# Performance work log

Measured on AMD Instinct MI355X. Metric: run time of the kernel, lower is better.

Reference implementation:

```python
import jax, jax.numpy as jnp
import numpy as np

N_NODES = 50000
N_EDGES = 800000
D_IN = 256
HID = 128
OUT = 64
NEG_SLOPE = 0.2  # PyG GATConv default leaky_relu slope
EPS = 1e-16      # PyG softmax denominator epsilon


def _gat_conv(x, src, dst, W_src, W_dst, att_src, att_dst, bias, n_nodes):
    """Single-head PyG GATConv with add_self_loops=False.
    Returns (out [N, C_out], alpha [E])."""
    h_src = x @ W_src                     # [N, C]
    h_dst = x @ W_dst                     # [N, C]
    a_src = h_src @ att_src               # [N]
    a_dst = h_dst @ att_dst               # [N]
    logits = jax.nn.leaky_relu(a_src[src] + a_dst[dst], NEG_SLOPE)  # [E]
    # segment softmax over incoming edges of each dst node
    m = jax.ops.segment_max(logits, dst, num_segments=n_nodes)      # [N]
    e = jnp.exp(logits - m[dst])                                    # [E]
    denom = jax.ops.segment_sum(e, dst, num_segments=n_nodes)       # [N]
    alpha = e / (denom[dst] + EPS)                                  # [E]
    msg = h_src[src] * alpha[:, None]                               # [E, C]
    out = jax.ops.segment_sum(msg, dst, num_segments=n_nodes) + bias
    return out, alpha


def setup_inputs() -> dict:
    key = jax.random.key(0)
    ks = jax.random.split(key, 16)
    s = 0.05
    x = jax.random.normal(ks[0], (N_NODES, D_IN), dtype=jnp.float32)
    edge_index = jax.random.randint(ks[1], (2, N_EDGES), 0, N_NODES, dtype=jnp.int64)
    return {
        "x": x,
        "edge_index": edge_index,
        "W_src1": jax.random.normal(ks[2], (D_IN, HID), jnp.float32) * s,
        "W_dst1": jax.random.normal(ks[3], (D_IN, HID), jnp.float32) * s,
        "att_src1": jax.random.normal(ks[4], (HID,), jnp.float32) * s,
        "att_dst1": jax.random.normal(ks[5], (HID,), jnp.float32) * s,
        "b1": jnp.zeros((HID,), jnp.float32),
        "W_lin1": jax.random.normal(ks[6], (D_IN, HID), jnp.float32) * s,
        "b_lin1": jnp.zeros((HID,), jnp.float32),
        "W_src2": jax.random.normal(ks[7], (HID, OUT), jnp.float32) * s,
        "W_dst2": jax.random.normal(ks[8], (HID, OUT), jnp.float32) * s,
        "att_src2": jax.random.normal(ks[9], (OUT,), jnp.float32) * s,
        "att_dst2": jax.random.normal(ks[10], (OUT,), jnp.float32) * s,
        "b2": jnp.zeros((OUT,), jnp.float32),
        "W_lin2": jax.random.normal(ks[11], (HID, OUT), jnp.float32) * s,
        "b_lin2": jnp.zeros((OUT,), jnp.float32),
    }


def reference(x, edge_index, W_src1, W_dst1, att_src1, att_dst1, b1, W_lin1, b_lin1,
              W_src2, W_dst2, att_src2, att_dst2, b2, W_lin2, b_lin2):
    src, dst = edge_index[0], edge_index[1]
    n = x.shape[0]
    h, _ = _gat_conv(x, src, dst, W_src1, W_dst1, att_src1, att_dst1, b1, n)
    h = h + x @ W_lin1 + b_lin1
    h = jax.nn.relu(h)
    out, alpha = _gat_conv(h, src, dst, W_src2, W_dst2, att_src2, att_dst2, b2, n)
    out = out + h @ W_lin2 + b_lin2
    return out, alpha
```

## Files before the change

### kernel.cpp

```cpp
#include <hip/hip_runtime.h>
#include <math.h>

#define D_IN 256
#define HID 128
#define D_OUT 64
#define NEG_SLOPE 0.2f

#define NBUCK 196
#define BCAP  5120
#define P1_EPB 8192

typedef short short8 __attribute__((ext_vector_type(8)));
typedef float floatx4 __attribute__((ext_vector_type(4)));

__device__ __forceinline__ float wave_reduce_sum(float v) {
    #pragma unroll
    for (int off = 32; off > 0; off >>= 1) v += __shfl_xor(v, off, 64);
    return v;
}
__device__ __forceinline__ int wave_scan_incl_i(int v) {
    int lane = threadIdx.x & 63;
    #pragma unroll
    for (int off = 1; off < 64; off <<= 1) {
        int t = __shfl_up(v, off, 64);
        if (lane >= off) v += t;
    }
    return v;
}

__device__ __forceinline__ short f2bf(float f) {
    unsigned u = __float_as_uint(f);
    u += 0x7fffu + ((u >> 16) & 1u);
    return (short)(u >> 16);
}
__device__ __forceinline__ unsigned pk2(float a, float b) {
    return (unsigned)(unsigned short)f2bf(a) | ((unsigned)(unsigned short)f2bf(b) << 16);
}
__device__ __forceinline__ float bflo(unsigned p) { return __uint_as_float(p << 16); }
__device__ __forceinline__ float bfhi(unsigned p) { return __uint_as_float(p & 0xffff0000u); }

__device__ void prep_body(const float* Wsrc1, const float* att_src1,
                          const float* Wdst1, const float* att_dst1,
                          const float* Wsrc2, const float* att_src2,
                          const float* Wdst2, const float* att_dst2,
                          const float* b1, const float* b_lin1,
                          const float* b2, const float* b_lin2,
                          float* v_src1, float* v_dst1, float* v_src2, float* v_dst2,
                          float* bsum1, float* bsum2) {
    int t = threadIdx.x;
    if (t < D_IN) {
        float s1 = 0.f, s2 = 0.f;
        for (int c = 0; c < HID; c++) {
            s1 += Wsrc1[t * HID + c] * att_src1[c];
            s2 += Wdst1[t * HID + c] * att_dst1[c];
        }
        v_src1[t] = s1; v_dst1[t] = s2;
    }
    if (t < HID) {
        float s1 = 0.f, s2 = 0.f;
        for (int c = 0; c < D_OUT; c++) {
            s1 += Wsrc2[t * D_OUT + c] * att_src2[c];
            s2 += Wdst2[t * D_OUT + c] * att_dst2[c];
        }
        v_src2[t] = s1; v_dst2[t] = s2;
        bsum1[t] = b1[t] + b_lin1[t];
    }
    if (t < D_OUT) bsum2[t] = b2[t] + b_lin2[t];
}

__device__ void pack_body(const float* Wa, const float* Wb, short* Wp,
                          int NTG, int NH, int total, int idx) {
    if (idx >= total) return;
    int j = idx & 7;
    int lane = (idx >> 3) & 63;
    int r = idx >> 9;
    int nt = r % NTG;
    int s = r / NTG;
    int k = s * 32 + ((lane >> 4) * 8) + j;
    int cg = nt * 16 + (lane & 15);
    const float* W = (cg < NH) ? Wa : Wb;
    int col = (cg < NH) ? cg : cg - NH;
    Wp[idx] = f2bf(W[(size_t)k * NH + col]);
}

__device__ void bucket_scatter_body(const int* __restrict__ src, const int* __restrict__ dst,
                                    int E, int* bcur, unsigned* ebuf, int blk) {
    __shared__ int hist[NBUCK];
    __shared__ int gbase[NBUCK];
    int t = threadIdx.x;
    for (int i = t; i < NBUCK; i += 256) hist[i] = 0;
    __syncthreads();
    int e0 = blk * P1_EPB;
    int e1 = e0 + P1_EPB; if (e1 > E) e1 = E;
    for (int e = e0 + t; e < e1; e += 256)
        atomicAdd(&hist[dst[e] >> 8], 1);
    __syncthreads();
    for (int i = t; i < NBUCK; i += 256) {
        gbase[i] = atomicAdd(&bcur[i], hist[i]);
        hist[i] = 0;
    }
    __syncthreads();
    for (int e = e0 + t; e < e1; e += 256) {
        int d = dst[e];
        int b = d >> 8;
        int slot = atomicAdd(&hist[b], 1);
        int pos = gbase[b] + slot;
        if (pos < BCAP)
            ebuf[(size_t)b * BCAP + pos] = (unsigned)src[e] | ((unsigned)(d & 255) << 16);
    }
}

__global__ void fused_pre(const int* __restrict__ src, const int* __restrict__ dst, int E,
                          int* bcur, unsigned* ebuf, int P1B,
                          const float* W_src1, const float* W_lin1, short* Wp1,
                          const float* W_src2, const float* W_lin2, short* Wp2,
                          const float* att_src1, const float* W_dst1, const float* att_dst1,
                          const float* att_src2, const float* W_dst2, const float* att_dst2,
                          const float* b1, const float* b_lin1,
                          const float* b2, const float* b_lin2,
                          float* v_src1, float* v_dst1, float* v_src2, float* v_dst2,
                          float* bsum1, float* bsum2) {
    int bid = blockIdx.x;
    if (bid < P1B) {
        bucket_scatter_body(src, dst, E, bcur, ebuf, bid);
    } else if (bid < P1B + 256) {
        pack_body(W_src1, W_lin1, Wp1, 16, HID, 8 * 16 * 512, (bid - P1B) * 256 + threadIdx.x);
    } else if (bid < P1B + 320) {
        pack_body(W_src2, W_lin2, Wp2, 8, D_OUT, 4 * 8 * 512, (bid - P1B - 256) * 256 + threadIdx.x);
    } else {
        prep_body(W_src1, att_src1, W_dst1, att_dst1, W_src2, att_src2, W_dst2, att_dst2,
                  b1, b_lin1, b2, b_lin2, v_src1, v_dst1, v_src2, v_dst2, bsum1, bsum2);
    }
}

__device__ void build_csr_body(const int* __restrict__ bcur, const unsigned* __restrict__ ebuf,
                               int* __restrict__ ssrc, int* __restrict__ row_beg,
                               int* __restrict__ row_end, int Nn, int b) {
    __shared__ int cnt[256];
    __shared__ int ofs[256];
    __shared__ int wsum[4];
    int t = threadIdx.x;
    cnt[t] = 0;
    __syncthreads();
    int n = bcur[b]; if (n > BCAP) n = BCAP;
    const unsigned* eb = ebuf + (size_t)b * BCAP;
    for (int i = t; i < n; i += 256)
        atomicAdd(&cnt[eb[i] >> 16], 1);
    __syncthreads();
    int v = cnt[t];
    int incl = wave_scan_incl_i(v);
    if ((t & 63) == 63) wsum[t >> 6] = incl;
    __syncthreads();
    int add = 0;
    #pragma unroll
    for (int w = 0; w < 4; w++) if (w < (t >> 6)) add += wsum[w];
    int excl = add + incl - v;
    int base = b * BCAP;
    int node = b * 256 + t;
    if (node < Nn) { row_beg[node] = base + excl; row_end[node] = base + excl + v; }
    ofs[t] = base + excl;
    __syncthreads();
    for (int i = t; i < n; i += 256) {
        unsigned r = eb[i];
        int pos = atomicAdd(&ofs[r >> 16], 1);
        ssrc[pos] = (int)(r & 0xffffu);
    }
}

__global__ void fused_mid(const int* __restrict__ bcur, const unsigned* __restrict__ ebuf,
                          int* ssrc, int* row_beg, int* row_end,
                          const float* __restrict__ X,
                          const float* __restrict__ vsrc, const float* __restrict__ vdst,
                          unsigned short* __restrict__ xb,
                          float* __restrict__ a_src, float* __restrict__ a_dst, int Nn) {
    int bid = blockIdx.x;
    if (bid < NBUCK) {
        build_csr_body(bcur, ebuf, ssrc, row_beg, row_end, Nn, bid);
    } else {
        int row = (bid - NBUCK) * 4 + (threadIdx.x >> 6);
        int lane = threadIdx.x & 63;
        if (row >= Nn) return;
        float4 v = *(const float4*)(X + (size_t)row * D_IN + lane * 4);
        float4 vs = *(const float4*)(vsrc + lane * 4);
        float4 vd = *(const float4*)(vdst + lane * 4);
        float ps = v.x * vs.x + v.y * vs.y + v.z * vs.z + v.w * vs.w;
        float pd = v.x * vd.x + v.y * vd.y + v.z * vd.z + v.w * vd.w;
        ushort4 o;
        o.x = (unsigned short)f2bf(v.x); o.y = (unsigned short)f2bf(v.y);
        o.z = (unsigned short)f2bf(v.z); o.w = (unsigned short)f2bf(v.w);
        *(ushort4*)(xb + (size_t)row * D_IN + lane * 4) = o;
        ps = wave_reduce_sum(ps);
        pd = wave_reduce_sum(pd);
        if (lane == 0) { a_src[row] = ps; a_dst[row] = pd; }
    }
}

template <int KS, int NT>
__global__ __launch_bounds__(256, 3) void gemm_direct(const unsigned short* __restrict__ A,
                                                      const short* __restrict__ Wp,
                                                      const float* __restrict__ bias,
                                                      unsigned short* __restrict__ outb,
                                                      unsigned short* __restrict__ outc, int M) {
    const int K = KS * 32;
    const int NTG = 4 * NT;
    const int NH = NT * 32;
    int tid = threadIdx.x;
    int wave = tid >> 6, lane = tid & 63;
    int mr = lane & 15, quad = lane >> 4;
    int bm = blockIdx.x * 64;

    floatx4 acc[4][NT];
    #pragma unroll
    for (int i = 0; i < 4; i++)
        #pragma unroll
        for (int j = 0; j < NT; j++) acc[i][j] = (floatx4){0.f, 0.f, 0.f, 0.f};

    const unsigned short* arow[4];
    #pragma unroll
    for (int tm = 0; tm < 4; tm++) {
        int gr = bm + tm * 16 + mr;
        if (gr >= M) gr = M - 1;
        arow[tm] = A + (size_t)gr * K + quad * 8;
    }
    const short* bbase = Wp + ((size_t)(wave * NT) * 64 + lane) * 8;

    #pragma unroll
    for (int s = 0; s < KS; s++) {
        short8 af[4], bf[NT];
        #pragma unroll
        for (int tm = 0; tm < 4; tm++)
            af[tm] = *(const short8*)(arow[tm] + s * 32);
        #pragma unroll
        for (int tn = 0; tn < NT; tn++)
            bf[tn] = *(const short8*)(bbase + ((size_t)s * NTG + tn) * 512);
        #pragma unroll
        for (int tn = 0; tn < NT; tn++)
            #pragma unroll
            for (int tm = 0; tm < 4; tm++)
                acc[tm][tn] = __builtin_amdgcn_mfma_f32_16x16x32_bf16(af[tm], bf[tn],
                                                                      acc[tm][tn], 0, 0, 0);
    }

    #pragma unroll
    for (int tm = 0; tm < 4; tm++) {
        #pragma unroll
        for (int tn = 0; tn < NT; tn++) {
            int cg = wave * NT * 16 + tn * 16 + mr;
            if (cg < NH) {
                #pragma unroll
                for (int r = 0; r < 4; r++) {
                    int gr = bm + tm * 16 + quad * 4 + r;
                    if (gr < M)
                        outb[(size_t)gr * NH + cg] = (unsigned short)f2bf(acc[tm][tn][r]);
                }
            } else {
                float bv = bias[cg - NH];
                #pragma unroll
                for (int r = 0; r < 4; r++) {
                    int gr = bm + tm * 16 + quad * 4 + r;
                    if (gr < M)
                        outc[(size_t)gr * NH + (cg - NH)] = (unsigned short)f2bf(acc[tm][tn][r] + bv);
                }
            }
        }
    }
}

__global__ void agg1_kernel(const int* __restrict__ row_beg, const int* __restrict__ row_end,
                            const int* __restrict__ ssrc,
                            const float* __restrict__ a_src, const float* __restrict__ a_dst,
                            const unsigned short* __restrict__ h1b,
                            const unsigned short* __restrict__ linb,
                            const float* __restrict__ vs2, const float* __restrict__ vd2,
                            unsigned short* __restrict__ hb,
                            float* __restrict__ a_src2, float* __restrict__ a_dst2, int Nn) {
    int node = blockIdx.x * 4 + (threadIdx.x >> 6);
    int lane = threadIdx.x & 63;
    if (node >= Nn) return;
    int beg = row_beg[node], end = row_end[node];
    float ad = a_dst[node];

    int qh = lane >> 4, cl = lane & 15;
    float acc[8] = {0.f, 0.f, 0.f, 0.f, 0.f, 0.f, 0.f, 0.f};
    float dsum = 0.f;
    const unsigned short* hcol = h1b + cl * 8;
    int j = beg + qh;
    for (; j + 4 < end; j += 8) {
        int s0 = ssrc[j], s1 = ssrc[j + 4];
        float l0 = a_src[s0] + ad; l0 = (l0 > 0.f) ? l0 : NEG_SLOPE * l0;
        float l1 = a_src[s1] + ad; l1 = (l1 > 0.f) ? l1 : NEG_SLOPE * l1;
        float w0 = __expf(l0), w1 = __expf(l1);
        uint4 p0 = *(const uint4*)(hcol + (size_t)s0 * HID);
        uint4 p1 = *(const uint4*)(hcol + (size_t)s1 * HID);
        acc[0] += w0 * bflo(p0.x); acc[1] += w0 * bfhi(p0.x);
        acc[2] += w0 * bflo(p0.y); acc[3] += w0 * bfhi(p0.y);
        acc[4] += w0 * bflo(p0.z); acc[5] += w0 * bfhi(p0.z);
        acc[6] += w0 * bflo(p0.w); acc[7] += w0 * bfhi(p0.w);
        acc[0] += w1 * bflo(p1.x); acc[1] += w1 * bfhi(p1.x);
        acc[2] += w1 * bflo(p1.y); acc[3] += w1 * bfhi(p1.y);
        acc[4] += w1 * bflo(p1.z); acc[5] += w1 * bfhi(p1.z);
        acc[6] += w1 * bflo(p1.w); acc[7] += w1 * bfhi(p1.w);
        if (cl == 0) dsum += w0 + w1;
    }
    for (; j < end; j += 4) {
        int s0 = ssrc[j];
        float l = a_src[s0] + ad; l = (l > 0.f) ? l : NEG_SLOPE * l;
        float w = __expf(l);
        uint4 p = *(const uint4*)(hcol + (size_t)s0 * HID);
        acc[0] += w * bflo(p.x); acc[1] += w * bfhi(p.x);
        acc[2] += w * bflo(p.y); acc[3] += w * bfhi(p.y);
        acc[4] += w * bflo(p.z); acc[5] += w * bfhi(p.z);
        acc[6] += w * bflo(p.w); acc[7] += w * bfhi(p.w);
        if (cl == 0) dsum += w;
    }
    #pragma unroll
    for (int i = 0; i < 8; i++) {
        acc[i] += __shfl_xor(acc[i], 16, 64);
        acc[i] += __shfl_xor(acc[i], 32, 64);
    }
    dsum = wave_reduce_sum(dsum);
    float inv = 1.f / (dsum + 1e-16f);

    int c = cl * 8;
    uint4 lb = *(const uint4*)(linb + (size_t)node * HID + c);
    float o[8];
    o[0] = fmaxf(acc[0] * inv + bflo(lb.x), 0.f);
    o[1] = fmaxf(acc[1] * inv + bfhi(lb.x), 0.f);
    o[2] = fmaxf(acc[2] * inv + bflo(lb.y), 0.f);
    o[3] = fmaxf(acc[3] * inv + bfhi(lb.y), 0.f);
    o[4] = fmaxf(acc[4] * inv + bflo(lb.z), 0.f);
    o[5] = fmaxf(acc[5] * inv + bfhi(lb.z), 0.f);
    o[6] = fmaxf(acc[6] * inv + bflo(lb.w), 0.f);
    o[7] = fmaxf(acc[7] * inv + bfhi(lb.w), 0.f);
    if (qh == 0) {
        uint4 pk;
        pk.x = pk2(o[0], o[1]); pk.y = pk2(o[2], o[3]);
        pk.z = pk2(o[4], o[5]); pk.w = pk2(o[6], o[7]);
        *(uint4*)&hb[(size_t)node * HID + c] = pk;
    }
    float ps = 0.f, pd = 0.f;
    #pragma unroll
    for (int i = 0; i < 8; i++) { ps += o[i] * vs2[c + i]; pd += o[i] * vd2[c + i]; }
    ps = wave_reduce_sum(ps) * 0.25f;
    pd = wave_reduce_sum(pd) * 0.25f;
    if (lane == 0) { a_src2[node] = ps; a_dst2[node] = pd; }
}

__global__ void agg2_kernel(const int* __restrict__ row_beg, const int* __restrict__ row_end,
                            const int* __restrict__ ssrc,
                            const float* __restrict__ a_src, const float* __restrict__ a_dst,
                            const unsigned short* __restrict__ h2b,
                            const unsigned short* __restrict__ lin2b,
                            float* __restrict__ out, float* __restrict__ sminv, int Nn) {
    int node = blockIdx.x * 4 + (threadIdx.x >> 6);
    int lane = threadIdx.x & 63;
    if (node >= Nn) return;
    int beg = row_beg[node], end = row_end[node];
    float ad = a_dst[node];

    int oh = lane >> 3, cl = lane & 7;
    float acc[8] = {0.f, 0.f, 0.f, 0.f, 0.f, 0.f, 0.f, 0.f};
    float dsum = 0.f;
    const unsigned short* hcol = h2b + cl * 8;
    int j = beg + oh;
    for (; j + 8 < end; j += 16) {
        int s0 = ssrc[j], s1 = ssrc[j + 8];
        float l0 = a_src[s0] + ad; l0 = (l0 > 0.f) ? l0 : NEG_SLOPE * l0;
        float l1 = a_src[s1] + ad; l1 = (l1 > 0.f) ? l1 : NEG_SLOPE * l1;
        float w0 = __expf(l0), w1 = __expf(l1);
        uint4 p0 = *(const uint4*)(hcol + (size_t)s0 * D_OUT);
        uint4 p1 = *(const uint4*)(hcol + (size_t)s1 * D_OUT);
        acc[0] += w0 * bflo(p0.x); acc[1] += w0 * bfhi(p0.x);
        acc[2] += w0 * bflo(p0.y); acc[3] += w0 * bfhi(p0.y);
        acc[4] += w0 * bflo(p0.z); acc[5] += w0 * bfhi(p0.z);
        acc[6] += w0 * bflo(p0.w); acc[7] += w0 * bfhi(p0.w);
        acc[0] += w1 * bflo(p1.x); acc[1] += w1 * bfhi(p1.x);
        acc[2] += w1 * bflo(p1.y); acc[3] += w1 * bfhi(p1.y);
        acc[4] += w1 * bflo(p1.z); acc[5] += w1 * bfhi(p1.z);
        acc[6] += w1 * bflo(p1.w); acc[7] += w1 * bfhi(p1.w);
        if (cl == 0) dsum += w0 + w1;
    }
    for (; j < end; j += 8) {
        int s0 = ssrc[j];
        float l = a_src[s0] + ad; l = (l > 0.f) ? l : NEG_SLOPE * l;
        float w = __expf(l);
        uint4 p = *(const uint4*)(hcol + (size_t)s0 * D_OUT);
        acc[0] += w * bflo(p.x); acc[1] += w * bfhi(p.x);
        acc[2] += w * bflo(p.y); acc[3] += w * bfhi(p.y);
        acc[4] += w * bflo(p.z); acc[5] += w * bfhi(p.z);
        acc[6] += w * bflo(p.w); acc[7] += w * bfhi(p.w);
        if (cl == 0) dsum += w;
    }
    #pragma unroll
    for (int i = 0; i < 8; i++) {
        acc[i] += __shfl_xor(acc[i], 8, 64);
        acc[i] += __shfl_xor(acc[i], 16, 64);
        acc[i] += __shfl_xor(acc[i], 32, 64);
    }
    dsum = wave_reduce_sum(dsum);
    float inv = 1.f / (dsum + 1e-16f);
    if (lane == 0) sminv[node] = inv;

    if (oh == 0) {
        int c = cl * 8;
        uint4 lb = *(const uint4*)(lin2b + (size_t)node * D_OUT + c);
        float4 oa = make_float4(acc[0] * inv + bflo(lb.x), acc[1] * inv + bfhi(lb.x),
                                acc[2] * inv + bflo(lb.y), acc[3] * inv + bfhi(lb.y));
        float4 ob = make_float4(acc[4] * inv + bflo(lb.z), acc[5] * inv + bfhi(lb.z),
                                acc[6] * inv + bflo(lb.w), acc[7] * inv + bfhi(lb.w));
        *(float4*)&out[(size_t)node * D_OUT + c] = oa;
        *(float4*)&out[(size_t)node * D_OUT + c + 4] = ob;
    }
}

__global__ void alpha_kernel(const int* __restrict__ src, const int* __restrict__ dst,
                             const float* __restrict__ a_src2, const float* __restrict__ a_dst2,
                             const float* __restrict__ sminv, float* __restrict__ alpha, int E) {
    int e = blockIdx.x * 256 + threadIdx.x;
    if (e >= E) return;
    int s = src[e], d = dst[e];
    float l = a_src2[s] + a_dst2[d];
    l = (l > 0.f) ? l : NEG_SLOPE * l;
    alpha[e] = __expf(l) * sminv[d];
}

extern "C" void kernel_launch(void* const* d_in, const int* in_sizes, int n_in,
                              void* d_out, int out_size, void* d_ws, size_t ws_size,
                              hipStream_t stream) {
    const float* x        = (const float*)d_in[0];
    const int*   ei       = (const int*)d_in[1];
    const float* W_src1   = (const float*)d_in[2];
    const float* W_dst1   = (const float*)d_in[3];
    const float* att_src1 = (const float*)d_in[4];
    const float* att_dst1 = (const float*)d_in[5];
    const float* b1       = (const float*)d_in[6];
    const float* W_lin1   = (const float*)d_in[7];
    const float* b_lin1   = (const float*)d_in[8];
    const float* W_src2   = (const float*)d_in[9];
    const float* W_dst2   = (const float*)d_in[10];
    const float* att_src2 = (const float*)d_in[11];
    const float* att_dst2 = (const float*)d_in[12];
    const float* b2       = (const float*)d_in[13];
    const float* W_lin2   = (const float*)d_in[14];
    const float* b_lin2   = (const float*)d_in[15];

    const int Nn = in_sizes[0] / D_IN;
    const int E  = in_sizes[1] / 2;
    const int* src = ei;
    const int* dst = ei + E;

    char* w = (char*)d_ws;
    auto alloc = [&](size_t bytes) { char* p = w; w += (bytes + 255) & ~(size_t)255; return p; };
    unsigned short* xb   = (unsigned short*)alloc((size_t)Nn * D_IN * 2);
    unsigned short* h1b  = (unsigned short*)alloc((size_t)Nn * HID * 2);
    unsigned short* lin1b= (unsigned short*)alloc((size_t)Nn * HID * 2);
    unsigned short* hb   = (unsigned short*)alloc((size_t)Nn * HID * 2);
    unsigned short* h2b  = (unsigned short*)alloc((size_t)Nn * D_OUT * 2);
    unsigned short* lin2b= (unsigned short*)alloc((size_t)Nn * D_OUT * 2);
    float* a_src1 = (float*)alloc((size_t)Nn * 4);
    float* a_dst1 = (float*)alloc((size_t)Nn * 4);
    float* a_src2 = (float*)alloc((size_t)Nn * 4);
    float* a_dst2 = (float*)alloc((size_t)Nn * 4);
    float* sminv  = (float*)alloc((size_t)Nn * 4);
    int*   row_beg= (int*)alloc((size_t)Nn * 4);
    int*   row_end= (int*)alloc((size_t)Nn * 4);
    int*   bcur   = (int*)alloc((size_t)NBUCK * 4);
    unsigned* ebuf= (unsigned*)alloc((size_t)NBUCK * BCAP * 4);
    int*   ssrc   = (int*)alloc((size_t)NBUCK * BCAP * 4);
    short* Wp1    = (short*)alloc((size_t)8 * 16 * 512 * 2);
    short* Wp2    = (short*)alloc((size_t)4 * 8 * 512 * 2);
    float* v_src1 = (float*)alloc(D_IN * 4);
    float* v_dst1 = (float*)alloc(D_IN * 4);
    float* v_src2 = (float*)alloc(HID * 4);
    float* v_dst2 = (float*)alloc(HID * 4);
    float* bsum1  = (float*)alloc(HID * 4);
    float* bsum2  = (float*)alloc(D_OUT * 4);

    float* out       = (float*)d_out;
    float* alpha_out = out + (size_t)Nn * D_OUT;

    hipMemsetAsync(bcur, 0, (size_t)NBUCK * 4, stream);

    int P1B = (E + P1_EPB - 1) / P1_EPB;
    fused_pre<<<P1B + 321, 256, 0, stream>>>(src, dst, E, bcur, ebuf, P1B,
                                             W_src1, W_lin1, Wp1, W_src2, W_lin2, Wp2,
                                             att_src1, W_dst1, att_dst1,
                                             att_src2, W_dst2, att_dst2,
                                             b1, b_lin1, b2, b_lin2,
                                             v_src1, v_dst1, v_src2, v_dst2, bsum1, bsum2);

    int ablocks = (Nn + 3) / 4;
    fused_mid<<<NBUCK + ablocks, 256, 0, stream>>>(bcur, ebuf, ssrc, row_beg, row_end,
                                                   x, v_src1, v_dst1, xb, a_src1, a_dst1, Nn);

    int mblocks = (Nn + 63) / 64;
    gemm_direct<8, 4><<<mblocks, 256, 0, stream>>>(xb, Wp1, bsum1, h1b, lin1b, Nn);

    agg1_kernel<<<ablocks, 256, 0, stream>>>(row_beg, row_end, ssrc, a_src1, a_dst1, h1b, lin1b,
                                             v_src2, v_dst2, hb, a_src2, a_dst2, Nn);

    gemm_direct<4, 2><<<mblocks, 256, 0, stream>>>(hb, Wp2, bsum2, h2b, lin2b, Nn);
    agg2_kernel<<<ablocks, 256, 0, stream>>>(row_beg, row_end, ssrc, a_src2, a_dst2, h2b, lin2b,
                                             out, sminv, Nn);
    int eblocks = (E + 255) / 256;
    alpha_kernel<<<eblocks, 256, 0, stream>>>(src, dst, a_src2, a_dst2, sminv, alpha_out, E);
}
```

Before: 277.0 us.

## Reschedule stages: move bf16 conversion into pre kernel, fuse GEMM1 with CSR build

```diff
diff --git a/kernel.cpp b/kernel.cpp
--- a/kernel.cpp
+++ b/kernel.cpp
@@ -110,6 +110,18 @@
     }
 }
 
+__device__ void convert_body(const float* __restrict__ X, unsigned short* __restrict__ xb,
+                             int Nn, int rb) {
+    int row = rb * 4 + (threadIdx.x >> 6);
+    int lane = threadIdx.x & 63;
+    if (row >= Nn) return;
+    float4 v = *(const float4*)(X + (size_t)row * D_IN + lane * 4);
+    ushort4 o;
+    o.x = (unsigned short)f2bf(v.x); o.y = (unsigned short)f2bf(v.y);
+    o.z = (unsigned short)f2bf(v.z); o.w = (unsigned short)f2bf(v.w);
+    *(ushort4*)(xb + (size_t)row * D_IN + lane * 4) = o;
+}
+
 __global__ void fused_pre(const int* __restrict__ src, const int* __restrict__ dst, int E,
                           int* bcur, unsigned* ebuf, int P1B,
                           const float* W_src1, const float* W_lin1, short* Wp1,
@@ -119,7 +131,8 @@
                           const float* b1, const float* b_lin1,
                           const float* b2, const float* b_lin2,
                           float* v_src1, float* v_dst1, float* v_src2, float* v_dst2,
-                          float* bsum1, float* bsum2) {
+                          float* bsum1, float* bsum2,
+                          const float* __restrict__ X, unsigned short* __restrict__ xb, int Nn) {
     int bid = blockIdx.x;
     if (bid < P1B) {
         bucket_scatter_body(src, dst, E, bcur, ebuf, bid);
@@ -127,9 +140,11 @@
         pack_body(W_src1, W_lin1, Wp1, 16, HID, 8 * 16 * 512, (bid - P1B) * 256 + threadIdx.x);
     } else if (bid < P1B + 320) {
         pack_body(W_src2, W_lin2, Wp2, 8, D_OUT, 4 * 8 * 512, (bid - P1B - 256) * 256 + threadIdx.x);
-    } else {
+    } else if (bid < P1B + 321) {
         prep_body(W_src1, att_src1, W_dst1, att_dst1, W_src2, att_src2, W_dst2, att_dst2,
                   b1, b_lin1, b2, b_lin2, v_src1, v_dst1, v_src2, v_dst2, bsum1, bsum2);
+    } else {
+        convert_body(X, xb, Nn, bid - (P1B + 321));
     }
 }
 
@@ -167,47 +182,36 @@
     }
 }
 
-__global__ void fused_mid(const int* __restrict__ bcur, const unsigned* __restrict__ ebuf,
-                          int* ssrc, int* row_beg, int* row_end,
-                          const float* __restrict__ X,
+__device__ void dots_body(const unsigned short* __restrict__ xb,
                           const float* __restrict__ vsrc, const float* __restrict__ vdst,
-                          unsigned short* __restrict__ xb,
-                          float* __restrict__ a_src, float* __restrict__ a_dst, int Nn) {
-    int bid = blockIdx.x;
-    if (bid < NBUCK) {
-        build_csr_body(bcur, ebuf, ssrc, row_beg, row_end, Nn, bid);
-    } else {
-        int row = (bid - NBUCK) * 4 + (threadIdx.x >> 6);
-        int lane = threadIdx.x & 63;
-        if (row >= Nn) return;
-        float4 v = *(const float4*)(X + (size_t)row * D_IN + lane * 4);
-        float4 vs = *(const float4*)(vsrc + lane * 4);
-        float4 vd = *(const float4*)(vdst + lane * 4);
-        float ps = v.x * vs.x + v.y * vs.y + v.z * vs.z + v.w * vs.w;
-        float pd = v.x * vd.x + v.y * vd.y + v.z * vd.z + v.w * vd.w;
-        ushort4 o;
-        o.x = (unsigned short)f2bf(v.x); o.y = (unsigned short)f2bf(v.y);
-        o.z = (unsigned short)f2bf(v.z); o.w = (unsigned short)f2bf(v.w);
-        *(ushort4*)(xb + (size_t)row * D_IN + lane * 4) = o;
-        ps = wave_reduce_sum(ps);
-        pd = wave_reduce_sum(pd);
-        if (lane == 0) { a_src[row] = ps; a_dst[row] = pd; }
-    }
+                          float* __restrict__ a_src, float* __restrict__ a_dst,
+                          int Nn, int rb) {
+    int row = rb * 4 + (threadIdx.x >> 6);
+    int lane = threadIdx.x & 63;
+    if (row >= Nn) return;
+    uint2 p = *(const uint2*)(xb + (size_t)row * D_IN + lane * 4);
+    float4 vs = *(const float4*)(vsrc + lane * 4);
+    float4 vd = *(const float4*)(vdst + lane * 4);
+    float x0 = bflo(p.x), x1 = bfhi(p.x), x2 = bflo(p.y), x3 = bfhi(p.y);
+    float ps = x0 * vs.x + x1 * vs.y + x2 * vs.z + x3 * vs.w;
+    float pd = x0 * vd.x + x1 * vd.y + x2 * vd.z + x3 * vd.w;
+    ps = wave_reduce_sum(ps);
+    pd = wave_reduce_sum(pd);
+    if (lane == 0) { a_src[row] = ps; a_dst[row] = pd; }
 }
 
 template <int KS, int NT>
-__global__ __launch_bounds__(256, 3) void gemm_direct(const unsigned short* __restrict__ A,
-                                                      const short* __restrict__ Wp,
-                                                      const float* __restrict__ bias,
-                                                      unsigned short* __restrict__ outb,
-                                                      unsigned short* __restrict__ outc, int M) {
+__device__ void gemm_body(const unsigned short* __restrict__ A,
+                          const short* __restrict__ Wp,
+                          const float* __restrict__ bias,
+                          unsigned short* __restrict__ outb,
+                          unsigned short* __restrict__ outc, int M, int bm) {
     const int K = KS * 32;
     const int NTG = 4 * NT;
     const int NH = NT * 32;
     int tid = threadIdx.x;
     int wave = tid >> 6, lane = tid & 63;
     int mr = lane & 15, quad = lane >> 4;
-    int bm = blockIdx.x * 64;
 
     floatx4 acc[4][NT];
     #pragma unroll
@@ -264,6 +268,37 @@
             }
         }
     }
+}
+
+__global__ __launch_bounds__(256, 3) void fused_g1(const unsigned short* __restrict__ xb,
+                                                   const short* __restrict__ Wp1,
+                                                   const float* __restrict__ bsum1,
+                                                   unsigned short* __restrict__ h1b,
+                                                   unsigned short* __restrict__ lin1b,
+                                                   int M, int MB,
+                                                   const int* __restrict__ bcur,
+                                                   const unsigned* __restrict__ ebuf,
+                                                   int* ssrc, int* row_beg, int* row_end, int Nn,
+                                                   const float* __restrict__ v_src1,
+                                                   const float* __restrict__ v_dst1,
+                                                   float* a_src1, float* a_dst1) {
+    int bid = blockIdx.x;
+    if (bid < MB) {
+        gemm_body<8, 4>(xb, Wp1, bsum1, h1b, lin1b, M, bid * 64);
+    } else if (bid < MB + NBUCK) {
+        build_csr_body(bcur, ebuf, ssrc, row_beg, row_end, Nn, bid - MB);
+    } else {
+        dots_body(xb, v_src1, v_dst1, a_src1, a_dst1, Nn, bid - MB - NBUCK);
+    }
+}
+
+template <int KS, int NT>
+__global__ __launch_bounds__(256, 3) void gemm_direct(const unsigned short* __restrict__ A,
+                                                      const short* __restrict__ Wp,
+                                                      const float* __restrict__ bias,
+                                                      unsigned short* __restrict__ outb,
+                                                      unsigned short* __restrict__ outc, int M) {
+    gemm_body<KS, NT>(A, Wp, bias, outb, outc, M, blockIdx.x * 64);
 }
 
 __global__ void agg1_kernel(const int* __restrict__ row_beg, const int* __restrict__ row_end,
@@ -482,19 +517,20 @@
     hipMemsetAsync(bcur, 0, (size_t)NBUCK * 4, stream);
 
     int P1B = (E + P1_EPB - 1) / P1_EPB;
-    fused_pre<<<P1B + 321, 256, 0, stream>>>(src, dst, E, bcur, ebuf, P1B,
+    int ablocks = (Nn + 3) / 4;
+    fused_pre<<<P1B + 321 + ablocks, 256, 0, stream>>>(src, dst, E, bcur, ebuf, P1B,
                                              W_src1, W_lin1, Wp1, W_src2, W_lin2, Wp2,
                                              att_src1, W_dst1, att_dst1,
                                              att_src2, W_dst2, att_dst2,
                                              b1, b_lin1, b2, b_lin2,
-                                             v_src1, v_dst1, v_src2, v_dst2, bsum1, bsum2);
-
-    int ablocks = (Nn + 3) / 4;
-    fused_mid<<<NBUCK + ablocks, 256, 0, stream>>>(bcur, ebuf, ssrc, row_beg, row_end,
-                                                   x, v_src1, v_dst1, xb, a_src1, a_dst1, Nn);
+                                             v_src1, v_dst1, v_src2, v_dst2, bsum1, bsum2,
+                                             x, xb, Nn);
 
     int mblocks = (Nn + 63) / 64;
-    gemm_direct<8, 4><<<mblocks, 256, 0, stream>>>(xb, Wp1, bsum1, h1b, lin1b, Nn);
+    fused_g1<<<mblocks + NBUCK + ablocks, 256, 0, stream>>>(xb, Wp1, bsum1, h1b, lin1b, Nn,
+                                                            mblocks, bcur, ebuf, ssrc,
+                                                            row_beg, row_end, Nn,
+                                                            v_src1, v_dst1, a_src1, a_dst1);
 
     agg1_kernel<<<ablocks, 256, 0, stream>>>(row_beg, row_end, ssrc, a_src1, a_dst1, h1b, lin1b,
                                              v_src2, v_dst2, hb, a_src2, a_dst2, Nn);
```

New measurement: 275.5 us. Within noise of the previous version (-0.5%).
